# Optimization experiments

Measured on AMD Instinct MI355X. Metric: run time of the kernel, lower is better.

## Reference

```python
import jax, jax.numpy as jnp
import numpy as np

H, S, D = 64, 64, 4096  # num_heads, head_size, hidden_size (D = H*S)
EPS = 1e-5


def setup_inputs() -> dict:
    key = jax.random.key(0)
    ks = jax.random.split(key, 20)
    n = lambda i, shape, s=1.0: s * jax.random.normal(ks[i], shape, dtype=jnp.float32)
    u = lambda i, shape: jax.random.uniform(ks[i], shape, dtype=jnp.float32)
    return {
        "x": n(0, (D,)),
        "state1": n(1, (D,)),
        "state2": n(2, (H, S, S), 0.1),
        "time_mix_k": u(3, (D,)),
        "time_mix_v": u(4, (D,)),
        "time_mix_r": u(5, (D,)),
        "time_mix_g": u(6, (D,)),
        # time_decay = exp(-exp(raw)) in (0,1); time_first = exp(raw) (time_faaaa-style, kept small)
        "time_decay": jnp.exp(-jnp.exp(n(7, (H, S, 1), 0.5))),
        "time_first": 0.3 * u(8, (H, S, 1)),
        "Wr": n(9, (D, D), 0.02),
        "Wk": n(10, (D, D), 0.01),   # key.weight / 2 baked in
        "Wv": n(11, (D, D), 0.005),  # value.weight / 4 baked in
        "Wg": n(12, (D, D), 0.02),
        "Wo": n(13, (D, D), 0.02),
        "ln1_w": 1.0 + n(14, (D,), 0.1),
        "ln1_b": n(15, (D,), 0.1),
        "lnx_w": 1.0 + n(16, (D,), 0.1),
        "lnx_b": n(17, (D,), 0.1),
    }


def reference(x, state1, state2, time_mix_k, time_mix_v, time_mix_r, time_mix_g,
              time_decay, time_first, Wr, Wk, Wv, Wg, Wo,
              ln1_w, ln1_b, lnx_w, lnx_b):
    last_x = x
    # ln_1 (nn.LayerNorm affine is identity-init; explicit w/b applied after)
    m = jnp.mean(x)
    var = jnp.mean((x - m) ** 2)
    xx = (x - m) * jax.lax.rsqrt(var + EPS) * ln1_w + ln1_b
    state1_out = xx

    mix = lambda t: state1 * (1.0 - t) + xx * t
    r = (Wr @ mix(time_mix_r)).reshape(H, 1, S)
    k = (Wk @ mix(time_mix_k)).reshape(H, S, 1)
    v = (Wv @ mix(time_mix_v)).reshape(H, 1, S)
    g_lin = Wg @ mix(time_mix_g)
    gate = g_lin * jax.nn.sigmoid(g_lin)  # SiLU

    kv = jnp.matmul(k, v)                              # [H, S, S] outer products
    wkv = jnp.matmul(r, kv * time_first + state2)       # [H, 1, S]
    state2_out = kv + state2 * time_decay

    # InstanceNorm2d over (1, S) spatial dims per head, no affine, biased var
    mu = jnp.mean(wkv, axis=(1, 2), keepdims=True)
    vv = jnp.mean((wkv - mu) ** 2, axis=(1, 2), keepdims=True)
    xn = ((wkv - mu) * jax.lax.rsqrt(vv + EPS)).reshape(D)
    y = (xn * lnx_w + lnx_b) * gate
    out = last_x + Wo @ y
    return (out, state1_out, state2_out)
```

## Files before the change

### kernel.cpp

```cpp
#include <hip/hip_runtime.h>
#include <math.h>

#define D 4096
#define H 64
#define S 64
#define EPS 1e-5f

__device__ __forceinline__ float wave_reduce_sum(float v) {
#pragma unroll
    for (int off = 32; off > 0; off >>= 1) v += __shfl_down(v, off, 64);
    return v;
}

__global__ __launch_bounds__(1024) void k_ln_mix(
    const float* __restrict__ x, const float* __restrict__ state1,
    const float* __restrict__ tmk, const float* __restrict__ tmv,
    const float* __restrict__ tmr, const float* __restrict__ tmg,
    const float* __restrict__ ln1w, const float* __restrict__ ln1b,
    float* __restrict__ state1_out, float* __restrict__ mix ) {
    __shared__ float red[32];
    __shared__ float mb[2];
    const int tid = threadIdx.x;
    const float4 xv = ((const float4*)x)[tid];
    float s = (xv.x + xv.y) + (xv.z + xv.w);
    float sq = (xv.x * xv.x + xv.y * xv.y) + (xv.z * xv.z + xv.w * xv.w);
    s = wave_reduce_sum(s);
    sq = wave_reduce_sum(sq);
    const int wave = tid >> 6, lane = tid & 63;
    if (lane == 0) { red[wave] = s; red[16 + wave] = sq; }
    __syncthreads();
    if (tid == 0) {
        float ts = 0.f, tq = 0.f;
        for (int i = 0; i < 16; ++i) { ts += red[i]; tq += red[16 + i]; }
        float m = ts / (float)D;
        float var = tq / (float)D - m * m;
        mb[0] = m;
        mb[1] = rsqrtf(var + EPS);
    }
    __syncthreads();
    const float m = mb[0], rs = mb[1];
    const float4 w4 = ((const float4*)ln1w)[tid];
    const float4 b4 = ((const float4*)ln1b)[tid];
    float4 xx;
    xx.x = (xv.x - m) * rs * w4.x + b4.x;
    xx.y = (xv.y - m) * rs * w4.y + b4.y;
    xx.z = (xv.z - m) * rs * w4.z + b4.z;
    xx.w = (xv.w - m) * rs * w4.w + b4.w;
    ((float4*)state1_out)[tid] = xx;
    const float4 s1 = ((const float4*)state1)[tid];
    float4 d;
    d.x = xx.x - s1.x; d.y = xx.y - s1.y; d.z = xx.z - s1.z; d.w = xx.w - s1.w;
    const float4 tr = ((const float4*)tmr)[tid];
    const float4 tk = ((const float4*)tmk)[tid];
    const float4 tv = ((const float4*)tmv)[tid];
    const float4 tg = ((const float4*)tmg)[tid];
    float4 o;
    o.x = s1.x + d.x * tr.x; o.y = s1.y + d.y * tr.y; o.z = s1.z + d.z * tr.z; o.w = s1.w + d.w * tr.w;
    ((float4*)mix)[tid] = o;
    o.x = s1.x + d.x * tk.x; o.y = s1.y + d.y * tk.y; o.z = s1.z + d.z * tk.z; o.w = s1.w + d.w * tk.w;
    ((float4*)mix)[1024 + tid] = o;
    o.x = s1.x + d.x * tv.x; o.y = s1.y + d.y * tv.y; o.z = s1.z + d.z * tv.z; o.w = s1.w + d.w * tv.w;
    ((float4*)mix)[2048 + tid] = o;
    o.x = s1.x + d.x * tg.x; o.y = s1.y + d.y * tg.y; o.z = s1.z + d.z * tg.z; o.w = s1.w + d.w * tg.w;
    ((float4*)mix)[3072 + tid] = o;
}

__global__ __launch_bounds__(256) void k_gemv4(
    const float* __restrict__ Wr, const float* __restrict__ Wk,
    const float* __restrict__ Wv, const float* __restrict__ Wg,
    const float* __restrict__ mix, float* __restrict__ rkvg) {
    __shared__ float4 smix[1024];
    const int wave = threadIdx.x >> 6, lane = threadIdx.x & 63;
    const int wg = blockIdx.x * 4 + wave;
    const int m = wg >> 11;
    const int r0 = (wg & 2047) * 2;
    const float* W = (m == 0) ? Wr : (m == 1) ? Wk : (m == 2) ? Wv : Wg;
    const float4* vx = (const float4*)mix + (m << 10);
#pragma unroll
    for (int t = 0; t < 4; ++t) smix[t * 256 + threadIdx.x] = vx[t * 256 + threadIdx.x];
    __syncthreads();
    const float4* w0p = (const float4*)W + (size_t)r0 * 1024;
    const float4* w1p = w0p + 1024;
    float a0 = 0.f, a1 = 0.f, b0 = 0.f, b1 = 0.f;
#pragma unroll
    for (int half = 0; half < 2; ++half) {
        float4 wa[8], wb[8];
#pragma unroll
        for (int u = 0; u < 8; ++u) wa[u] = w0p[(half * 8 + u) * 64 + lane];
#pragma unroll
        for (int u = 0; u < 8; ++u) wb[u] = w1p[(half * 8 + u) * 64 + lane];
#pragma unroll
        for (int u = 0; u < 8; ++u) {
            float4 xv = smix[(half * 8 + u) * 64 + lane];
            a0 += wa[u].x * xv.x + wa[u].y * xv.y;
            a1 += wa[u].z * xv.z + wa[u].w * xv.w;
            b0 += wb[u].x * xv.x + wb[u].y * xv.y;
            b1 += wb[u].z * xv.z + wb[u].w * xv.w;
        }
    }
    float a = wave_reduce_sum(a0 + a1);
    float b = wave_reduce_sum(b0 + b1);
    if (lane == 0) {
        rkvg[m * D + r0] = a;
        rkvg[m * D + r0 + 1] = b;
    }
}

__global__ __launch_bounds__(1024) void k_heads(
    const float* __restrict__ rkvg, const float* __restrict__ state2,
    const float* __restrict__ tdecay, const float* __restrict__ tfirst,
    const float* __restrict__ lnxw, const float* __restrict__ lnxb,
    float* __restrict__ state2_out, float* __restrict__ y) {
    __shared__ float part[16][64];
    const int h = blockIdx.x;
    const int wave = threadIdx.x >> 6, j = threadIdx.x & 63;
    const int base = h * S;
    const float rj = rkvg[base + j];
    const float kj = rkvg[D + base + j];
    const float vj = rkvg[2 * D + base + j];
    const float tfj = tfirst[base + j];
    const float tdj = tdecay[base + j];
    const float* s2 = state2 + (size_t)h * S * S;
    float* s2o = state2_out + (size_t)h * S * S;
    float sv[4];
#pragma unroll
    for (int ii = 0; ii < 4; ++ii) sv[ii] = s2[(wave * 4 + ii) * S + j];
    float wkv = 0.f;
#pragma unroll
    for (int ii = 0; ii < 4; ++ii) {
        const int i = wave * 4 + ii;
        float ri = __shfl(rj, i, 64);
        float ki = __shfl(kj, i, 64);
        float tfi = __shfl(tfj, i, 64);
        float tdi = __shfl(tdj, i, 64);
        float kv = ki * vj;
        wkv += ri * (kv * tfi + sv[ii]);
        s2o[i * S + j] = kv + sv[ii] * tdi;
    }
    part[wave][j] = wkv;
    __syncthreads();
    if (wave == 0) {
        float w0 = 0.f;
#pragma unroll
        for (int t = 0; t < 16; ++t) w0 += part[t][j];
        float sum = w0, sq = w0 * w0;
#pragma unroll
        for (int off = 1; off < 64; off <<= 1) {
            sum += __shfl_xor(sum, off, 64);
            sq += __shfl_xor(sq, off, 64);
        }
        float mu = sum / (float)S;
        float var = sq / (float)S - mu * mu;
        float xn = (w0 - mu) * rsqrtf(var + EPS);
        float gj = rkvg[3 * D + base + j];
        float gate = gj / (1.f + expf(-gj));
        y[base + j] = (xn * lnxw[base + j] + lnxb[base + j]) * gate;
    }
}

__global__ __launch_bounds__(256) void k_out(
    const float* __restrict__ Wo, const float* __restrict__ y,
    const float* __restrict__ x, float* __restrict__ out) {
    __shared__ float4 sy[1024];
    const int wave = threadIdx.x >> 6, lane = threadIdx.x & 63;
    const int wg = blockIdx.x * 4 + wave;
    const int r0 = wg * 2;
    const float4* vy = (const float4*)y;
#pragma unroll
    for (int t = 0; t < 4; ++t) sy[t * 256 + threadIdx.x] = vy[t * 256 + threadIdx.x];
    __syncthreads();
    const float4* w0p = (const float4*)Wo + (size_t)r0 * 1024;
    const float4* w1p = w0p + 1024;
    float a0 = 0.f, a1 = 0.f, b0 = 0.f, b1 = 0.f;
#pragma unroll
    for (int half = 0; half < 2; ++half) {
        float4 wa[8], wb[8];
#pragma unroll
        for (int u = 0; u < 8; ++u) wa[u] = w0p[(half * 8 + u) * 64 + lane];
#pragma unroll
        for (int u = 0; u < 8; ++u) wb[u] = w1p[(half * 8 + u) * 64 + lane];
#pragma unroll
        for (int u = 0; u < 8; ++u) {
            float4 xv = sy[(half * 8 + u) * 64 + lane];
            a0 += wa[u].x * xv.x + wa[u].y * xv.y;
            a1 += wa[u].z * xv.z + wa[u].w * xv.w;
            b0 += wb[u].x * xv.x + wb[u].y * xv.y;
            b1 += wb[u].z * xv.z + wb[u].w * xv.w;
        }
    }
    float a = wave_reduce_sum(a0 + a1);
    float b = wave_reduce_sum(b0 + b1);
    if (lane == 0) {
        out[r0] = x[r0] + a;
        out[r0 + 1] = x[r0 + 1] + b;
    }
}

extern "C" void kernel_launch(void* const* d_in, const int* in_sizes, int n_in,
                              void* d_out, int out_size, void* d_ws, size_t ws_size,
                              hipStream_t stream) {
    const float* x      = (const float*)d_in[0];
    const float* state1 = (const float*)d_in[1];
    const float* state2 = (const float*)d_in[2];
    const float* tmk    = (const float*)d_in[3];
    const float* tmv    = (const float*)d_in[4];
    const float* tmr    = (const float*)d_in[5];
    const float* tmg    = (const float*)d_in[6];
    const float* tdecay = (const float*)d_in[7];
    const float* tfirst = (const float*)d_in[8];
    const float* Wr     = (const float*)d_in[9];
    const float* Wk     = (const float*)d_in[10];
    const float* Wv     = (const float*)d_in[11];
    const float* Wg     = (const float*)d_in[12];
    const float* Wo     = (const float*)d_in[13];
    const float* ln1w   = (const float*)d_in[14];
    const float* ln1b   = (const float*)d_in[15];
    const float* lnxw   = (const float*)d_in[16];
    const float* lnxb   = (const float*)d_in[17];

    float* out        = (float*)d_out;
    float* state1_out = out + D;
    float* state2_out = out + 2 * D;

    float* mix  = (float*)d_ws;
    float* rkvg = mix + 4 * D;
    float* y    = rkvg + 4 * D;

    k_ln_mix<<<1, 1024, 0, stream>>>(x, state1, tmk, tmv, tmr, tmg, ln1w, ln1b,
                                     state1_out, mix);
    k_gemv4<<<2048, 256, 0, stream>>>(Wr, Wk, Wv, Wg, mix, rkvg);
    k_heads<<<64, 1024, 0, stream>>>(rkvg, state2, tdecay, tfirst, lnxw, lnxb,
                                     state2_out, y);
    k_out<<<512, 256, 0, stream>>>(Wo, y, x, out);
}
```

Before: 320.3 us.

## Fuse all stages into one persistent kernel with software grid barriers

New measurement: 1.009 ms. 3.15x slower.

```diff
diff --git a/kernel.cpp b/kernel.cpp
--- a/kernel.cpp
+++ b/kernel.cpp
@@ -5,6 +5,7 @@
 #define H 64
 #define S 64
 #define EPS 1e-5f
+#define NB 1024
 
 __device__ __forceinline__ float wave_reduce_sum(float v) {
 #pragma unroll
@@ -12,188 +13,190 @@
     return v;
 }
 
-__global__ __launch_bounds__(1024) void k_ln_mix(
+__device__ __forceinline__ void grid_barrier(unsigned* cnt, unsigned* gen) {
+    __threadfence();
+    __syncthreads();
+    if (threadIdx.x == 0) {
+        unsigned g = __hip_atomic_load(gen, __ATOMIC_RELAXED, __HIP_MEMORY_SCOPE_AGENT);
+        unsigned t = __hip_atomic_fetch_add(cnt, 1u, __ATOMIC_ACQ_REL, __HIP_MEMORY_SCOPE_AGENT);
+        if (t == NB - 1u) {
+            __hip_atomic_store(cnt, 0u, __ATOMIC_RELAXED, __HIP_MEMORY_SCOPE_AGENT);
+            __hip_atomic_fetch_add(gen, 1u, __ATOMIC_RELEASE, __HIP_MEMORY_SCOPE_AGENT);
+        } else {
+            int guard = 0;
+            while (__hip_atomic_load(gen, __ATOMIC_ACQUIRE, __HIP_MEMORY_SCOPE_AGENT) == g
+                   && ++guard < (1 << 28)) { }
+        }
+    }
+    __syncthreads();
+    __threadfence();
+}
+
+__global__ __launch_bounds__(256, 4) void k_mega(
     const float* __restrict__ x, const float* __restrict__ state1,
+    const float* __restrict__ state2,
     const float* __restrict__ tmk, const float* __restrict__ tmv,
     const float* __restrict__ tmr, const float* __restrict__ tmg,
+    const float* __restrict__ tdecay, const float* __restrict__ tfirst,
+    const float* __restrict__ Wr, const float* __restrict__ Wk,
+    const float* __restrict__ Wv, const float* __restrict__ Wg,
+    const float* __restrict__ Wo,
     const float* __restrict__ ln1w, const float* __restrict__ ln1b,
-    float* __restrict__ state1_out, float* __restrict__ mix ) {
-    __shared__ float red[32];
+    const float* __restrict__ lnxw, const float* __restrict__ lnxb,
+    float* __restrict__ out, float* __restrict__ state1_out,
+    float* __restrict__ state2_out, float* __restrict__ rkvg,
+    float* __restrict__ y, unsigned* __restrict__ bar)
+{
+    __shared__ float4 smix[1024];
+    __shared__ float red[8];
     __shared__ float mb[2];
+    __shared__ float part[4][64];
+
     const int tid = threadIdx.x;
-    const float4 xv = ((const float4*)x)[tid];
-    float s = (xv.x + xv.y) + (xv.z + xv.w);
-    float sq = (xv.x * xv.x + xv.y * xv.y) + (xv.z * xv.z + xv.w * xv.w);
+    const int wave = tid >> 6, lane = tid & 63;
+    const int gb = blockIdx.x;
+    const int m = gb >> 8;
+    const int R = (gb & 255) * 16;
+
+    float4 x4[4];
+    float s = 0.f, sq = 0.f;
+#pragma unroll
+    for (int i = 0; i < 4; ++i) {
+        x4[i] = ((const float4*)x)[tid + 256 * i];
+        s  += (x4[i].x + x4[i].y) + (x4[i].z + x4[i].w);
+        sq += x4[i].x * x4[i].x + x4[i].y * x4[i].y
+            + x4[i].z * x4[i].z + x4[i].w * x4[i].w;
+    }
     s = wave_reduce_sum(s);
     sq = wave_reduce_sum(sq);
-    const int wave = tid >> 6, lane = tid & 63;
-    if (lane == 0) { red[wave] = s; red[16 + wave] = sq; }
+    if (lane == 0) { red[wave] = s; red[4 + wave] = sq; }
     __syncthreads();
     if (tid == 0) {
-        float ts = 0.f, tq = 0.f;
-        for (int i = 0; i < 16; ++i) { ts += red[i]; tq += red[16 + i]; }
-        float m = ts / (float)D;
-        float var = tq / (float)D - m * m;
-        mb[0] = m;
-        mb[1] = rsqrtf(var + EPS);
-    }
-    __syncthreads();
-    const float m = mb[0], rs = mb[1];
-    const float4 w4 = ((const float4*)ln1w)[tid];
-    const float4 b4 = ((const float4*)ln1b)[tid];
-    float4 xx;
-    xx.x = (xv.x - m) * rs * w4.x + b4.x;
-    xx.y = (xv.y - m) * rs * w4.y + b4.y;
-    xx.z = (xv.z - m) * rs * w4.z + b4.z;
-    xx.w = (xv.w - m) * rs * w4.w + b4.w;
-    ((float4*)state1_out)[tid] = xx;
-    const float4 s1 = ((const float4*)state1)[tid];
-    float4 d;
-    d.x = xx.x - s1.x; d.y = xx.y - s1.y; d.z = xx.z - s1.z; d.w = xx.w - s1.w;
-    const float4 tr = ((const float4*)tmr)[tid];
-    const float4 tk = ((const float4*)tmk)[tid];
-    const float4 tv = ((const float4*)tmv)[tid];
-    const float4 tg = ((const float4*)tmg)[tid];
-    float4 o;
-    o.x = s1.x + d.x * tr.x; o.y = s1.y + d.y * tr.y; o.z = s1.z + d.z * tr.z; o.w = s1.w + d.w * tr.w;
-    ((float4*)mix)[tid] = o;
-    o.x = s1.x + d.x * tk.x; o.y = s1.y + d.y * tk.y; o.z = s1.z + d.z * tk.z; o.w = s1.w + d.w * tk.w;
-    ((float4*)mix)[1024 + tid] = o;
-    o.x = s1.x + d.x * tv.x; o.y = s1.y + d.y * tv.y; o.z = s1.z + d.z * tv.z; o.w = s1.w + d.w * tv.w;
-    ((float4*)mix)[2048 + tid] = o;
-    o.x = s1.x + d.x * tg.x; o.y = s1.y + d.y * tg.y; o.z = s1.z + d.z * tg.z; o.w = s1.w + d.w * tg.w;
-    ((float4*)mix)[3072 + tid] = o;
-}
-
-__global__ __launch_bounds__(256) void k_gemv4(
-    const float* __restrict__ Wr, const float* __restrict__ Wk,
-    const float* __restrict__ Wv, const float* __restrict__ Wg,
-    const float* __restrict__ mix, float* __restrict__ rkvg) {
-    __shared__ float4 smix[1024];
-    const int wave = threadIdx.x >> 6, lane = threadIdx.x & 63;
-    const int wg = blockIdx.x * 4 + wave;
-    const int m = wg >> 11;
-    const int r0 = (wg & 2047) * 2;
+        float ts = red[0] + red[1] + red[2] + red[3];
+        float tq = red[4] + red[5] + red[6] + red[7];
+        float mmean = ts / (float)D;
+        float var = tq / (float)D - mmean * mmean;
+        mb[0] = mmean; mb[1] = rsqrtf(var + EPS);
+    }
+    __syncthreads();
+    const float mmean = mb[0], rs = mb[1];
+    const float* tm = (m == 0) ? tmr : (m == 1) ? tmk : (m == 2) ? tmv : tmg;
+#pragma unroll
+    for (int i = 0; i < 4; ++i) {
+        const int idx = tid + 256 * i;
+        const float4 w4 = ((const float4*)ln1w)[idx];
+        const float4 b4 = ((const float4*)ln1b)[idx];
+        const float4 s1 = ((const float4*)state1)[idx];
+        const float4 t4 = ((const float4*)tm)[idx];
+        float4 xx;
+        xx.x = (x4[i].x - mmean) * rs * w4.x + b4.x;
+        xx.y = (x4[i].y - mmean) * rs * w4.y + b4.y;
+        xx.z = (x4[i].z - mmean) * rs * w4.z + b4.z;
+        xx.w = (x4[i].w - mmean) * rs * w4.w + b4.w;
+        if (gb == 0) ((float4*)state1_out)[idx] = xx;
+        float4 o;
+        o.x = s1.x + (xx.x - s1.x) * t4.x;
+        o.y = s1.y + (xx.y - s1.y) * t4.y;
+        o.z = s1.z + (xx.z - s1.z) * t4.z;
+        o.w = s1.w + (xx.w - s1.w) * t4.w;
+        smix[idx] = o;
+    }
+    __syncthreads();
+
     const float* W = (m == 0) ? Wr : (m == 1) ? Wk : (m == 2) ? Wv : Wg;
-    const float4* vx = (const float4*)mix + (m << 10);
-#pragma unroll
-    for (int t = 0; t < 4; ++t) smix[t * 256 + threadIdx.x] = vx[t * 256 + threadIdx.x];
-    __syncthreads();
-    const float4* w0p = (const float4*)W + (size_t)r0 * 1024;
-    const float4* w1p = w0p + 1024;
-    float a0 = 0.f, a1 = 0.f, b0 = 0.f, b1 = 0.f;
-#pragma unroll
-    for (int half = 0; half < 2; ++half) {
-        float4 wa[8], wb[8];
-#pragma unroll
-        for (int u = 0; u < 8; ++u) wa[u] = w0p[(half * 8 + u) * 64 + lane];
-#pragma unroll
-        for (int u = 0; u < 8; ++u) wb[u] = w1p[(half * 8 + u) * 64 + lane];
-#pragma unroll
-        for (int u = 0; u < 8; ++u) {
-            float4 xv = smix[(half * 8 + u) * 64 + lane];
-            a0 += wa[u].x * xv.x + wa[u].y * xv.y;
-            a1 += wa[u].z * xv.z + wa[u].w * xv.w;
-            b0 += wb[u].x * xv.x + wb[u].y * xv.y;
-            b1 += wb[u].z * xv.z + wb[u].w * xv.w;
-        }
-    }
-    float a = wave_reduce_sum(a0 + a1);
-    float b = wave_reduce_sum(b0 + b1);
+    const int r0 = R + wave * 4;
+    const float4* wp = (const float4*)W + (size_t)r0 * 1024;
+    float a0 = 0.f, a1 = 0.f, a2 = 0.f, a3 = 0.f;
+#pragma unroll
+    for (int c0 = 0; c0 < 16; c0 += 4) {
+        float4 w0[4], w1[4], w2[4], w3[4];
+#pragma unroll
+        for (int c = 0; c < 4; ++c) w0[c] = wp[(c0 + c) * 64 + lane];
+#pragma unroll
+        for (int c = 0; c < 4; ++c) w1[c] = wp[1024 + (c0 + c) * 64 + lane];
+#pragma unroll
+        for (int c = 0; c < 4; ++c) w2[c] = wp[2048 + (c0 + c) * 64 + lane];
+#pragma unroll
+        for (int c = 0; c < 4; ++c) w3[c] = wp[3072 + (c0 + c) * 64 + lane];
+#pragma unroll
+        for (int c = 0; c < 4; ++c) {
+            const float4 xv = smix[(c0 + c) * 64 + lane];
+            a0 += w0[c].x * xv.x + w0[c].y * xv.y + w0[c].z * xv.z + w0[c].w * xv.w;
+            a1 += w1[c].x * xv.x + w1[c].y * xv.y + w1[c].z * xv.z + w1[c].w * xv.w;
+            a2 += w2[c].x * xv.x + w2[c].y * xv.y + w2[c].z * xv.z + w2[c].w * xv.w;
+            a3 += w3[c].x * xv.x + w3[c].y * xv.y + w3[c].z * xv.z + w3[c].w * xv.w;
+        }
+    }
+    a0 = wave_reduce_sum(a0);
+    a1 = wave_reduce_sum(a1);
+    a2 = wave_reduce_sum(a2);
+    a3 = wave_reduce_sum(a3);
     if (lane == 0) {
-        rkvg[m * D + r0] = a;
-        rkvg[m * D + r0 + 1] = b;
-    }
-}
-
-__global__ __launch_bounds__(1024) void k_heads(
-    const float* __restrict__ rkvg, const float* __restrict__ state2,
-    const float* __restrict__ tdecay, const float* __restrict__ tfirst,
-    const float* __restrict__ lnxw, const float* __restrict__ lnxb,
-    float* __restrict__ state2_out, float* __restrict__ y) {
-    __shared__ float part[16][64];
-    const int h = blockIdx.x;
-    const int wave = threadIdx.x >> 6, j = threadIdx.x & 63;
-    const int base = h * S;
-    const float rj = rkvg[base + j];
-    const float kj = rkvg[D + base + j];
-    const float vj = rkvg[2 * D + base + j];
-    const float tfj = tfirst[base + j];
-    const float tdj = tdecay[base + j];
-    const float* s2 = state2 + (size_t)h * S * S;
-    float* s2o = state2_out + (size_t)h * S * S;
-    float sv[4];
-#pragma unroll
-    for (int ii = 0; ii < 4; ++ii) sv[ii] = s2[(wave * 4 + ii) * S + j];
-    float wkv = 0.f;
-#pragma unroll
-    for (int ii = 0; ii < 4; ++ii) {
-        const int i = wave * 4 + ii;
-        float ri = __shfl(rj, i, 64);
-        float ki = __shfl(kj, i, 64);
-        float tfi = __shfl(tfj, i, 64);
-        float tdi = __shfl(tdj, i, 64);
-        float kv = ki * vj;
-        wkv += ri * (kv * tfi + sv[ii]);
-        s2o[i * S + j] = kv + sv[ii] * tdi;
-    }
-    part[wave][j] = wkv;
-    __syncthreads();
-    if (wave == 0) {
-        float w0 = 0.f;
-#pragma unroll
-        for (int t = 0; t < 16; ++t) w0 += part[t][j];
-        float sum = w0, sq = w0 * w0;
-#pragma unroll
-        for (int off = 1; off < 64; off <<= 1) {
-            sum += __shfl_xor(sum, off, 64);
-            sq += __shfl_xor(sq, off, 64);
-        }
-        float mu = sum / (float)S;
-        float var = sq / (float)S - mu * mu;
-        float xn = (w0 - mu) * rsqrtf(var + EPS);
-        float gj = rkvg[3 * D + base + j];
-        float gate = gj / (1.f + expf(-gj));
-        y[base + j] = (xn * lnxw[base + j] + lnxb[base + j]) * gate;
-    }
-}
-
-__global__ __launch_bounds__(256) void k_out(
-    const float* __restrict__ Wo, const float* __restrict__ y,
-    const float* __restrict__ x, float* __restrict__ out) {
-    __shared__ float4 sy[1024];
-    const int wave = threadIdx.x >> 6, lane = threadIdx.x & 63;
-    const int wg = blockIdx.x * 4 + wave;
-    const int r0 = wg * 2;
-    const float4* vy = (const float4*)y;
-#pragma unroll
-    for (int t = 0; t < 4; ++t) sy[t * 256 + threadIdx.x] = vy[t * 256 + threadIdx.x];
-    __syncthreads();
-    const float4* w0p = (const float4*)Wo + (size_t)r0 * 1024;
-    const float4* w1p = w0p + 1024;
-    float a0 = 0.f, a1 = 0.f, b0 = 0.f, b1 = 0.f;
-#pragma unroll
-    for (int half = 0; half < 2; ++half) {
-        float4 wa[8], wb[8];
-#pragma unroll
-        for (int u = 0; u < 8; ++u) wa[u] = w0p[(half * 8 + u) * 64 + lane];
-#pragma unroll
-        for (int u = 0; u < 8; ++u) wb[u] = w1p[(half * 8 + u) * 64 + lane];
-#pragma unroll
-        for (int u = 0; u < 8; ++u) {
-            float4 xv = sy[(half * 8 + u) * 64 + lane];
-            a0 += wa[u].x * xv.x + wa[u].y * xv.y;
-            a1 += wa[u].z * xv.z + wa[u].w * xv.w;
-            b0 += wb[u].x * xv.x + wb[u].y * xv.y;
-            b1 += wb[u].z * xv.z + wb[u].w * xv.w;
-        }
-    }
-    float a = wave_reduce_sum(a0 + a1);
-    float b = wave_reduce_sum(b0 + b1);
-    if (lane == 0) {
-        out[r0] = x[r0] + a;
-        out[r0 + 1] = x[r0 + 1] + b;
-    }
+        float* dst = rkvg + m * D + r0;
+        dst[0] = a0; dst[1] = a1; dst[2] = a2; dst[3] = a3;
+    }
+
+    grid_barrier(bar, bar + 1);
+
+    if (gb < H) {
+        const int h = gb, j = lane;
+        const int base = h * S;
+        const float rj  = rkvg[base + j];
+        const float kj  = rkvg[D + base + j];
+        const float vj  = rkvg[2 * D + base + j];
+        const float tfj = tfirst[base + j];
+        const float tdj = tdecay[base + j];
+        const float* s2 = state2 + (size_t)h * S * S;
+        float* s2o = state2_out + (size_t)h * S * S;
+        float sv[16];
+#pragma unroll
+        for (int ii = 0; ii < 16; ++ii) sv[ii] = s2[(wave * 16 + ii) * S + j];
+        float wkv = 0.f;
+#pragma unroll
+        for (int ii = 0; ii < 16; ++ii) {
+            const int i = wave * 16 + ii;
+            const float ri  = __shfl(rj, i, 64);
+            const float ki  = __shfl(kj, i, 64);
+            const float tfi = __shfl(tfj, i, 64);
+            const float tdi = __shfl(tdj, i, 64);
+            const float kv = ki * vj;
+            wkv += ri * (kv * tfi + sv[ii]);
+            s2o[i * S + j] = kv + sv[ii] * tdi;
+        }
+        part[wave][j] = wkv;
+        __syncthreads();
+        if (wave == 0) {
+            const float w0 = part[0][j] + part[1][j] + part[2][j] + part[3][j];
+            float sum = w0, sq2 = w0 * w0;
+#pragma unroll
+            for (int off = 1; off < 64; off <<= 1) {
+                sum += __shfl_xor(sum, off, 64);
+                sq2 += __shfl_xor(sq2, off, 64);
+            }
+            const float mu = sum / (float)S;
+            const float var = sq2 / (float)S - mu * mu;
+            const float xn = (w0 - mu) * rsqrtf(var + EPS);
+            const float gj = rkvg[3 * D + base + j];
+            const float gate = gj / (1.f + expf(-gj));
+            y[base + j] = (xn * lnxw[base + j] + lnxb[base + j]) * gate;
+        }
+    }
+
+    grid_barrier(bar, bar + 1);
+
+    const int row = gb * 4 + wave;
+    const float4* wo = (const float4*)Wo + (size_t)row * 1024;
+    const float4* y4 = (const float4*)y;
+    float acc = 0.f;
+#pragma unroll 4
+    for (int c = 0; c < 16; ++c) {
+        const int o = c * 64 + lane;
+        const float4 yv = y4[o];
+        const float4 wv = wo[o];
+        acc += wv.x * yv.x + wv.y * yv.y + wv.z * yv.z + wv.w * yv.w;
+    }
+    acc = wave_reduce_sum(acc);
+    if (lane == 0) out[row] = x[row] + acc;
 }
 
 extern "C" void kernel_launch(void* const* d_in, const int* in_sizes, int n_in,
@@ -222,14 +225,14 @@
     float* state1_out = out + D;
     float* state2_out = out + 2 * D;
 
-    float* mix  = (float*)d_ws;
-    float* rkvg = mix + 4 * D;
+    float* rkvg = (float*)d_ws;
     float* y    = rkvg + 4 * D;
-
-    k_ln_mix<<<1, 1024, 0, stream>>>(x, state1, tmk, tmv, tmr, tmg, ln1w, ln1b,
-                                     state1_out, mix);
-    k_gemv4<<<2048, 256, 0, stream>>>(Wr, Wk, Wv, Wg, mix, rkvg);
-    k_heads<<<64, 1024, 0, stream>>>(rkvg, state2, tdecay, tfirst, lnxw, lnxb,
-                                     state2_out, y);
-    k_out<<<512, 256, 0, stream>>>(Wo, y, x, out);
-}
+    unsigned* bar = (unsigned*)(y + D);
+
+    hipMemsetAsync((void*)bar, 0, 2 * sizeof(unsigned), stream);
+
+    hipLaunchKernelGGL(k_mega, dim3(NB), dim3(256), 0, stream,
+                       x, state1, state2, tmk, tmv, tmr, tmg, tdecay, tfirst,
+                       Wr, Wk, Wv, Wg, Wo, ln1w, ln1b, lnxw, lnxb,
+                       out, state1_out, state2_out, rkvg, y, bar);
+}
```

## Stream GEMV weight rows through per-wave LDS ring with direct global-to-LDS loads

Applied to the files above, without the earlier changes.

Result: no change. 319.3 us (-0.3%).

```diff
diff --git a/kernel.cpp b/kernel.cpp
--- a/kernel.cpp
+++ b/kernel.cpp
@@ -11,6 +11,15 @@
     for (int off = 32; off > 0; off >>= 1) v += __shfl_down(v, off, 64);
     return v;
 }
+
+__device__ __forceinline__ void gl2lds16(const float* gbase, int lane, float* lds_slot) {
+    __builtin_amdgcn_global_load_lds(
+        (const __attribute__((address_space(1))) void*)(gbase + lane * 4),
+        (__attribute__((address_space(3))) void*)lds_slot, 16, 0, 0);
+}
+
+#define WAITV(N) asm volatile("s_waitcnt vmcnt(" #N ")" ::: "memory")
+#define WAITL()  asm volatile("s_waitcnt lgkmcnt(0)" ::: "memory")
 
 __global__ __launch_bounds__(1024) void k_ln_mix(
     const float* __restrict__ x, const float* __restrict__ state1,
@@ -65,11 +74,49 @@
     ((float4*)mix)[3072 + tid] = o;
 }
 
+#define GSTEP(C, VC, ISSUE)                                                     \
+    {                                                                           \
+        WAITV(VC);                                                              \
+        __builtin_amdgcn_sched_barrier(0);                                      \
+        const float4 w0 = ((const float4*)ring[wave][((C) & 3) * 2])[lane];     \
+        const float4 w1 = ((const float4*)ring[wave][((C) & 3) * 2 + 1])[lane]; \
+        const float4 xv = ((const float4*)svec)[(C) * 64 + lane];               \
+        WAITL();                \
+        __builtin_amdgcn_sched_barrier(0);                                      \
+        if (ISSUE) {                                                            \
+            gl2lds16(w0base + ((C) + 4) * 256, lane, &ring[wave][((C) & 3) * 2][0]);     \
+            gl2lds16(w1base + ((C) + 4) * 256, lane, &ring[wave][((C) & 3) * 2 + 1][0]); \
+        }                                                                       \
+        a0 += w0.x * xv.x + w0.y * xv.y;                                        \
+        a1 += w0.z * xv.z + w0.w * xv.w;                                        \
+        b0 += w1.x * xv.x + w1.y * xv.y;                                        \
+        b1 += w1.z * xv.z + w1.w * xv.w;                                        \
+    }
+
+#define GRUN()            \
+    GSTEP(0, 6, 1)        \
+    GSTEP(1, 6, 1)        \
+    GSTEP(2, 6, 1)        \
+    GSTEP(3, 6, 1)        \
+    GSTEP(4, 6, 1)        \
+    GSTEP(5, 6, 1)        \
+    GSTEP(6, 6, 1)        \
+    GSTEP(7, 6, 1)        \
+    GSTEP(8, 6, 1)        \
+    GSTEP(9, 6, 1)        \
+    GSTEP(10, 6, 1)       \
+    GSTEP(11, 6, 1)       \
+    GSTEP(12, 6, 0)       \
+    GSTEP(13, 4, 0)       \
+    GSTEP(14, 2, 0)       \
+    GSTEP(15, 0, 0)
+
 __global__ __launch_bounds__(256) void k_gemv4(
     const float* __restrict__ Wr, const float* __restrict__ Wk,
     const float* __restrict__ Wv, const float* __restrict__ Wg,
     const float* __restrict__ mix, float* __restrict__ rkvg) {
-    __shared__ float4 smix[1024];
+    __shared__ float4 svec[1024];
+    __shared__ float ring[4][8][256];
     const int wave = threadIdx.x >> 6, lane = threadIdx.x & 63;
     const int wg = blockIdx.x * 4 + wave;
     const int m = wg >> 11;
@@ -77,27 +124,19 @@
     const float* W = (m == 0) ? Wr : (m == 1) ? Wk : (m == 2) ? Wv : Wg;
     const float4* vx = (const float4*)mix + (m << 10);
 #pragma unroll
-    for (int t = 0; t < 4; ++t) smix[t * 256 + threadIdx.x] = vx[t * 256 + threadIdx.x];
-    __syncthreads();
-    const float4* w0p = (const float4*)W + (size_t)r0 * 1024;
-    const float4* w1p = w0p + 1024;
+    for (int t = 0; t < 4; ++t) svec[t * 256 + threadIdx.x] = vx[t * 256 + threadIdx.x];
+    __syncthreads();
+
+    const float* w0base = W + (size_t)r0 * D;
+    const float* w1base = w0base + D;
+#pragma unroll
+    for (int p = 0; p < 4; ++p) {
+        gl2lds16(w0base + p * 256, lane, &ring[wave][p * 2][0]);
+        gl2lds16(w1base + p * 256, lane, &ring[wave][p * 2 + 1][0]);
+    }
     float a0 = 0.f, a1 = 0.f, b0 = 0.f, b1 = 0.f;
-#pragma unroll
-    for (int half = 0; half < 2; ++half) {
-        float4 wa[8], wb[8];
-#pragma unroll
-        for (int u = 0; u < 8; ++u) wa[u] = w0p[(half * 8 + u) * 64 + lane];
-#pragma unroll
-        for (int u = 0; u < 8; ++u) wb[u] = w1p[(half * 8 + u) * 64 + lane];
-#pragma unroll
-        for (int u = 0; u < 8; ++u) {
-            float4 xv = smix[(half * 8 + u) * 64 + lane];
-            a0 += wa[u].x * xv.x + wa[u].y * xv.y;
-            a1 += wa[u].z * xv.z + wa[u].w * xv.w;
-            b0 += wb[u].x * xv.x + wb[u].y * xv.y;
-            b1 += wb[u].z * xv.z + wb[u].w * xv.w;
-        }
-    }
+    GRUN()
+
     float a = wave_reduce_sum(a0 + a1);
     float b = wave_reduce_sum(b0 + b1);
     if (lane == 0) {
@@ -161,33 +200,26 @@
 __global__ __launch_bounds__(256) void k_out(
     const float* __restrict__ Wo, const float* __restrict__ y,
     const float* __restrict__ x, float* __restrict__ out) {
-    __shared__ float4 sy[1024];
+    __shared__ float4 svec[1024];
+    __shared__ float ring[4][8][256];
     const int wave = threadIdx.x >> 6, lane = threadIdx.x & 63;
     const int wg = blockIdx.x * 4 + wave;
     const int r0 = wg * 2;
     const float4* vy = (const float4*)y;
 #pragma unroll
-    for (int t = 0; t < 4; ++t) sy[t * 256 + threadIdx.x] = vy[t * 256 + threadIdx.x];
-    __syncthreads();
-    const float4* w0p = (const float4*)Wo + (size_t)r0 * 1024;
-    const float4* w1p = w0p + 1024;
+    for (int t = 0; t < 4; ++t) svec[t * 256 + threadIdx.x] = vy[t * 256 + threadIdx.x];
+    __syncthreads();
+
+    const float* w0base = Wo + (size_t)r0 * D;
+    const float* w1base = w0base + D;
+#pragma unroll
+    for (int p = 0; p < 4; ++p) {
+        gl2lds16(w0base + p * 256, lane, &ring[wave][p * 2][0]);
+        gl2lds16(w1base + p * 256, lane, &ring[wave][p * 2 + 1][0]);
+    }
     float a0 = 0.f, a1 = 0.f, b0 = 0.f, b1 = 0.f;
-#pragma unroll
-    for (int half = 0; half < 2; ++half) {
-        float4 wa[8], wb[8];
-#pragma unroll
-        for (int u = 0; u < 8; ++u) wa[u] = w0p[(half * 8 + u) * 64 + lane];
-#pragma unroll
-        for (int u = 0; u < 8; ++u) wb[u] = w1p[(half * 8 + u) * 64 + lane];
-#pragma unroll
-        for (int u = 0; u < 8; ++u) {
-            float4 xv = sy[(half * 8 + u) * 64 + lane];
-            a0 += wa[u].x * xv.x + wa[u].y * xv.y;
-            a1 += wa[u].z * xv.z + wa[u].w * xv.w;
-            b0 += wb[u].x * xv.x + wb[u].y * xv.y;
-            b1 += wb[u].z * xv.z + wb[u].w * xv.w;
-        }
-    }
+    GRUN()
+
     float a = wave_reduce_sum(a0 + a1);
     float b = wave_reduce_sum(b0 + b1);
     if (lane == 0) {
```
